# Optimization experiments

Measured on AMD Instinct MI355X. Metric: run time of the kernel, lower is better.

Reference implementation:

```python
import jax, jax.numpy as jnp
import numpy as np

HEADS = 8
DK = 64   # key_size (defaults to size_per_head)
DV = 64   # size_per_head
RATE = 4
OUT = HEADS * DV  # 512


def extract_seq_patches(x, kernel, rate):
    # x: [b, L, d] -> [b, L, kernel, d]; strided local window gather
    b, L, d = x.shape
    k_size = kernel + (rate - 1) * (kernel - 1)
    p_right = (k_size - 1) // 2
    p_left = k_size - 1 - p_right
    xp = jnp.pad(x, ((0, 0), (p_left, p_right), (0, 0)))
    patches = [xp[:, i:i + L] for i in range(0, k_size, rate)]  # kernel slices
    return jnp.stack(patches, axis=2)


def setup_inputs() -> dict:
    key = jax.random.key(0)
    k1, k2, k3, k4 = jax.random.split(key, 4)
    s = 1.0 / np.sqrt(OUT)
    x = jax.random.normal(k1, (2, 4096, OUT), dtype=jnp.float32)
    Wq = jax.random.normal(k2, (OUT, HEADS * DK), dtype=jnp.float32) * s
    Wk = jax.random.normal(k3, (OUT, HEADS * DK), dtype=jnp.float32) * s
    Wv = jax.random.normal(k4, (OUT, HEADS * DV), dtype=jnp.float32) * s
    return {"x": x, "Wq": Wq, "Wk": Wk, "Wv": Wv}


def reference(x, Wq, Wk, Wv):
    b, L, d = x.shape
    pad = RATE - L % RATE  # torch code always pads (pad=RATE when L % RATE == 0)
    xpad = jnp.pad(x, ((0, 0), (0, pad), (0, 0)))
    nL = L + pad
    n = nL // RATE
    kernel = 2 * RATE - 1  # 1 + 2*neighbors

    qw = xpad @ Wq
    kw = xpad @ Wk
    vw = xpad @ Wv

    kwp = extract_seq_patches(kw, kernel, RATE)  # [b, nL, K, H*dk]
    vwp = extract_seq_patches(vw, kernel, RATE)  # [b, nL, K, H*dv]

    # [b, h, r, n, d]
    qw = qw.reshape(b, n, RATE, HEADS, DK).transpose(0, 3, 2, 1, 4)
    kw = kw.reshape(b, n, RATE, HEADS, DK).transpose(0, 3, 2, 1, 4)
    vw = vw.reshape(b, n, RATE, HEADS, DV).transpose(0, 3, 2, 1, 4)
    # [b, h, r, n, K, d]
    kwp = kwp.reshape(b, n, RATE, kernel, HEADS, DK).transpose(0, 4, 2, 1, 3, 5)
    vwp = vwp.reshape(b, n, RATE, kernel, HEADS, DV).transpose(0, 4, 2, 1, 3, 5)

    scale = 1.0 / np.sqrt(DK)
    a = jnp.einsum('bhrnd,bhrmd->bhrnm', qw, kw) * scale    # strided scores [b,h,r,n,n]
    ap = jnp.einsum('bhrnd,bhrnkd->bhrnk', qw, kwp) * scale  # local scores  [b,h,r,n,K]

    A = jax.nn.softmax(jnp.concatenate([a, ap], axis=-1), axis=-1)
    a, ap = A[..., :n], A[..., n:]

    o = jnp.einsum('bhrnm,bhrmd->bhrnd', a, vw) + jnp.einsum('bhrnk,bhrnkd->bhrnd', ap, vwp)
    o = o.transpose(0, 3, 2, 1, 4).reshape(b, nL, HEADS * DV)
    return o[:, :L]
```

## Files before the change

kernel.cpp:

```cpp
#include <hip/hip_runtime.h>
#include <hip/hip_bf16.h>


#define BATCH 2
#define LSEQ  4096
#define DMODEL 512
#define NH    8
#define DHEAD 64
#define NPAD  1088
#define QSCALE 0.18033688011112042f

typedef __bf16 bf16x8 __attribute__((ext_vector_type(8)));
typedef __attribute__((ext_vector_type(4))) float f32x4;
typedef unsigned short u16;
typedef unsigned int u32;
typedef __attribute__((ext_vector_type(8))) u16 u16x8;
typedef __attribute__((ext_vector_type(4))) u16 u16x4;

__device__ __forceinline__ u16 f2bf(float f) {
    u32 u = __float_as_uint(f);
    u += 0x7fffu + ((u >> 16) & 1u);
    return (u16)(u >> 16);
}

__device__ __forceinline__ void gload16(const u16* g, u16* l) {
    __builtin_amdgcn_global_load_lds(
        (const __attribute__((address_space(1))) u32*)(const void*)g,
        (__attribute__((address_space(3))) u32*)(void*)l, 16, 0, 0);
}

__global__ __launch_bounds__(256) void prep_kernel(
    const float* __restrict__ x,
    const float* __restrict__ Wq, const float* __restrict__ Wk, const float* __restrict__ Wv,
    u16* __restrict__ xb, u16* __restrict__ Wt,
    u16* __restrict__ Kb, u16* __restrict__ Vb)
{
    const int bid = blockIdx.x, tid = threadIdx.x;
    if (bid < 2048) {
        const size_t i0 = (size_t)bid * 2048 + (size_t)tid * 8;
        float4 a = *(const float4*)(x + i0);
        float4 b = *(const float4*)(x + i0 + 4);
        u16x8 o = { f2bf(a.x), f2bf(a.y), f2bf(a.z), f2bf(a.w),
                    f2bf(b.x), f2bf(b.y), f2bf(b.z), f2bf(b.w) };
        *(u16x8*)(xb + i0) = o;
    } else if (bid < 2240) {
        const int wb  = bid - 2048;
        const int mat = wb >> 6;
        const int t   = wb & 63;
        const int k0  = (t >> 3) * 64, c0 = (t & 7) * 64;
        const float* W = (mat == 0) ? Wq : (mat == 1) ? Wk : Wv;
        __shared__ u16 Ws[64][72];
        #pragma unroll
        for (int i = 0; i < 4; ++i) {
            const int chunk = i * 256 + tid;
            const int kr = chunk >> 4, c4 = (chunk & 15) * 4;
            float4 v = *(const float4*)(W + (size_t)(k0 + kr) * DMODEL + c0 + c4);
            u16x4 q = { f2bf(v.x), f2bf(v.y), f2bf(v.z), f2bf(v.w) };
            *(u16x4*)&Ws[kr][c4] = q;
        }
        __syncthreads();
        const int cc = tid >> 2, kq = (tid & 3) * 16;
        alignas(16) u16 tmp[16];
        #pragma unroll
        for (int kk = 0; kk < 16; ++kk) tmp[kk] = Ws[kq + kk][cc];
        u16* dst = Wt + (size_t)(mat * 512 + c0 + cc) * DMODEL + k0 + kq;
        *(u16x8*)dst       = *(const u16x8*)&tmp[0];
        *(u16x8*)(dst + 8) = *(const u16x8*)&tmp[8];
    } else {
        const int g = bid - 2240;
        const u16x8 z = {0,0,0,0,0,0,0,0};
        u16* kt = Kb + ((size_t)g * NPAD + 1024) * DHEAD + tid * 16;
        *(u16x8*)kt       = z;
        *(u16x8*)(kt + 8) = z;
        u16* vt = Vb + ((size_t)g * DHEAD + (tid >> 2)) * NPAD + 1024 + (tid & 3) * 16;
        *(u16x8*)vt       = z;
        *(u16x8*)(vt + 8) = z;
    }
}

__global__ __launch_bounds__(256) void gemm_kernel(
    const u16* __restrict__ xb, const u16* __restrict__ Wt,
    u16* __restrict__ Qb, u16* __restrict__ Kb, u16* __restrict__ Vb)
{
    const int m0 = blockIdx.x * 128;
    const int nt = blockIdx.y;
    const int n0 = nt * 128;
    const int tid = threadIdx.x;
    const int w = tid >> 6, l = tid & 63, lr = l & 15, lh = l >> 4;
    const int wr = w >> 1, wc = w & 1;

    __shared__ u16 smem[16896];
    u16* As = smem;
    u16* Bs = smem + 8192;

    f32x4 acc[4][4];
    const f32x4 fzero = {0.f, 0.f, 0.f, 0.f};
    #pragma unroll
    for (int mi = 0; mi < 4; ++mi)
        #pragma unroll
        for (int nj = 0; nj < 4; ++nj) acc[mi][nj] = fzero;

    for (int kt = 0; kt < 8; ++kt) {
        const int k0 = kt * 64;
        #pragma unroll
        for (int i = 0; i < 4; ++i) {
            const int cid = i * 256 + tid;
            const int row = cid >> 3, ch = cid & 7;
            const int sch = ch ^ (row & 7);
            u16* dstA = As + (i * 256 + w * 64) * 8;
            u16* dstB = Bs + (i * 256 + w * 64) * 8;
            gload16(xb + (size_t)(m0 + row) * DMODEL + k0 + sch * 8, dstA);
            gload16(Wt + (size_t)(n0 + row) * DMODEL + k0 + sch * 8, dstB);
        }
        __syncthreads();

        #pragma unroll
        for (int kk = 0; kk < 2; ++kk) {
            const int cs = (kk * 4 + lh) ^ (lr & 7);
            bf16x8 af[4], bfr[4];
            #pragma unroll
            for (int mi = 0; mi < 4; ++mi)
                af[mi] = *(const bf16x8*)(As + (wr * 64 + mi * 16 + lr) * 64 + cs * 8);
            #pragma unroll
            for (int nj = 0; nj < 4; ++nj)
                bfr[nj] = *(const bf16x8*)(Bs + (wc * 64 + nj * 16 + lr) * 64 + cs * 8);
            #pragma unroll
            for (int mi = 0; mi < 4; ++mi)
                #pragma unroll
                for (int nj = 0; nj < 4; ++nj)
                    acc[mi][nj] = __builtin_amdgcn_mfma_f32_16x16x32_bf16(af[mi], bfr[nj], acc[mi][nj], 0, 0, 0);
        }
        __syncthreads();
    }

    const int mat = nt >> 2;
    const int hp  = nt & 3;
    if (mat < 2) {
        u16* Ob = (mat == 0) ? Qb : Kb;
        const float osc = (mat == 0) ? QSCALE : 1.0f;
        #pragma unroll
        for (int mi = 0; mi < 4; ++mi) {
            const int gmb = m0 + wr * 64 + mi * 16 + lh * 4;
            const int b = gmb >> 12;
            #pragma unroll
            for (int rr = 0; rr < 4; ++rr) {
                const int t = (gmb + rr) & 4095;
                const int n = t >> 2, r = t & 3;
                #pragma unroll
                for (int nj = 0; nj < 4; ++nj) {
                    const int c  = wc * 64 + nj * 16 + lr;
                    const int h  = hp * 2 + (c >> 6);
                    const int dk = c & 63;
                    const size_t g = ((size_t)(b * NH + h)) * 4 + r;
                    Ob[(g * NPAD + n) * DHEAD + dk] = f2bf(acc[mi][nj][rr] * osc);
                }
            }
        }
    } else {
        #pragma unroll
        for (int mi = 0; mi < 4; ++mi) {
            const int nrel = wr * 16 + mi * 4 + lh;
            #pragma unroll
            for (int nj = 0; nj < 4; ++nj) {
                const int c = wc * 64 + nj * 16 + lr;
                #pragma unroll
                for (int rr = 0; rr < 4; ++rr)
                    smem[c * 132 + rr * 32 + nrel] = f2bf(acc[mi][nj][rr]);
            }
        }
        __syncthreads();
        const int b  = m0 >> 12;
        const int nb = (m0 & 4095) >> 2;
        #pragma unroll
        for (int e = 0; e < 2; ++e) {
            const int chunk = e * 256 + tid;
            const int c = chunk & 127, r = chunk >> 7;
            const int h  = hp * 2 + (c >> 6);
            const int dv = c & 63;
            const size_t g = ((size_t)(b * NH + h)) * 4 + r;
            u16* dst = Vb + (g * DHEAD + dv) * NPAD + nb;
            const u16* src = smem + c * 132 + r * 32;
            alignas(16) u16 tmp[32];
            #pragma unroll
            for (int q8 = 0; q8 < 8; ++q8)
                *(u16x4*)&tmp[q8 * 4] = *(const u16x4*)(src + q8 * 4);
            #pragma unroll
            for (int q16 = 0; q16 < 4; ++q16)
                *(u16x8*)(dst + q16 * 8) = *(const u16x8*)&tmp[q16 * 8];
        }
    }
}

__global__ __launch_bounds__(512) void attn_kernel(
    const u16* __restrict__ Qb, const u16* __restrict__ Kb, const u16* __restrict__ Vb,
    float* __restrict__ out)
{
    const int g  = blockIdx.x;
    const int b  = g >> 5;
    const int h  = (g >> 2) & 7;
    const int r  = g & 3;
    const int q0 = blockIdx.y * 128;
    const int tid = threadIdx.x;
    const int w  = tid >> 6;
    const int l  = tid & 63;
    const int lr = l & 15, lh = l >> 4;

    const u16* Qg  = Qb + (size_t)g * NPAD * DHEAD;
    const u16* Kg  = Kb + (size_t)g * NPAD * DHEAD;
    const u16* Vtg = Vb + (size_t)g * DHEAD * NPAD;

    __shared__ u16 KV[2][2][4096];
    __shared__ u16 Ps[8][16][68];

    const int srow = tid >> 3;
    const int ssch = (tid & 7) ^ (srow & 7);
    const u16* ksrc0 = Kg  + (size_t)srow * DHEAD + ssch * 8;
    const u16* vsrc0 = Vtg + (size_t)srow * NPAD  + ssch * 8;

    bf16x8 qa[2];
    {
        const u16* qrow = Qg + (size_t)(q0 + w * 16 + lr) * DHEAD;
        qa[0] = *(const bf16x8*)(qrow + lh * 8);
        qa[1] = *(const bf16x8*)(qrow + 32 + lh * 8);
    }

    const f32x4 fzero = {0.f, 0.f, 0.f, 0.f};
    f32x4 o[4];
    #pragma unroll
    for (int j = 0; j < 4; ++j) o[j] = fzero;
    float Lpart[4] = {0.f, 0.f, 0.f, 0.f};

    const int qw0 = q0 + w * 16;

    gload16(ksrc0, &KV[0][0][w * 512]);
    gload16(vsrc0 + 0, &KV[0][1][w * 512]);

    int cur = 0;
    for (int mt = 0; mt < 17; ++mt) {
        if (mt < 16) {
            gload16(ksrc0 + (size_t)(mt + 1) * 4096, &KV[cur ^ 1][0][w * 512]);
            gload16(vsrc0 + (mt + 1) * 64,           &KV[cur ^ 1][1][w * 512]);
            asm volatile("s_waitcnt vmcnt(2)" ::: "memory");
        } else {
            asm volatile("s_waitcnt vmcnt(0)" ::: "memory");
        }
        __builtin_amdgcn_s_barrier();

        const u16* Kbuf = KV[cur][0];
        const u16* Vbuf = KV[cur][1];

        f32x4 s[4];
        #pragma unroll
        for (int ni = 0; ni < 4; ++ni) {
            s[ni] = fzero;
            #pragma unroll
            for (int kk = 0; kk < 2; ++kk) {
                const int slot = (kk * 4 + lh) ^ (lr & 7);
                bf16x8 kb = *(const bf16x8*)(Kbuf + ((ni * 16 + lr) * 8 + slot) * 8);
                s[ni] = __builtin_amdgcn_mfma_f32_16x16x32_bf16(qa[kk], kb, s[ni], 0, 0, 0);
            }
        }

        const int m0 = mt * 64;
        const bool special = (mt == 16) || ((m0 + 66 >= qw0) && (m0 <= qw0 + 18));
        if (!special) {
            #pragma unroll
            for (int ni = 0; ni < 4; ++ni) {
                #pragma unroll
                for (int rr = 0; rr < 4; ++rr) {
                    const float p = __builtin_amdgcn_exp2f(s[ni][rr]);
                    Lpart[rr] += p;
                    Ps[w][lh * 4 + rr][ni * 16 + lr] = f2bf(p);
                }
            }
        } else {
            #pragma unroll
            for (int ni = 0; ni < 4; ++ni) {
                const int mg = m0 + ni * 16 + lr;
                #pragma unroll
                for (int rr = 0; rr < 4; ++rr) {
                    const int qg = qw0 + lh * 4 + rr;
                    float v = s[ni][rr];
                    const int dd = mg - qg;
                    if (mg > 1024)                 v = -1e30f;
                    else if (dd >= -3 && dd <= 3)  v += 1.0f;
                    const float p = __builtin_amdgcn_exp2f(v);
                    Lpart[rr] += p;
                    Ps[w][lh * 4 + rr][ni * 16 + lr] = f2bf(p);
                }
            }
        }

        #pragma unroll
        for (int kk = 0; kk < 2; ++kk) {
            bf16x8 pa = *(const bf16x8*)&Ps[w][lr][kk * 32 + lh * 8];
            #pragma unroll
            for (int j = 0; j < 4; ++j) {
                const int slot = (kk * 4 + lh) ^ (lr & 7);
                bf16x8 vb = *(const bf16x8*)(Vbuf + ((j * 16 + lr) * 8 + slot) * 8);
                o[j] = __builtin_amdgcn_mfma_f32_16x16x32_bf16(pa, vb, o[j], 0, 0, 0);
            }
        }
        __syncthreads();
        cur ^= 1;
    }

    #pragma unroll
    for (int rr = 0; rr < 4; ++rr) {
        float s_ = Lpart[rr];
        #pragma unroll
        for (int off = 1; off < 16; off <<= 1)
            s_ += __shfl_xor(s_, off, 16);
        const int qg = qw0 + lh * 4 + rr;
        const int coob = (qg < 3 ? 3 - qg : 0) + (qg > 1021 ? qg - 1021 : 0);
        const float inv = 1.0f / (s_ + (float)coob);
        const int t = qg * 4 + r;
        float* orow = out + ((size_t)b * LSEQ + t) * DMODEL + h * DHEAD;
        #pragma unroll
        for (int j = 0; j < 4; ++j)
            orow[j * 16 + lr] = o[j][rr] * inv;
    }
}

extern "C" void kernel_launch(void* const* d_in, const int* in_sizes, int n_in,
                              void* d_out, int out_size, void* d_ws, size_t ws_size,
                              hipStream_t stream) {
    const float* x  = (const float*)d_in[0];
    const float* Wq = (const float*)d_in[1];
    const float* Wk = (const float*)d_in[2];
    const float* Wv = (const float*)d_in[3];
    float* out = (float*)d_out;

    const size_t SZ = (size_t)BATCH * NH * 4 * NPAD * DHEAD;
    u16* Qb = (u16*)d_ws;
    u16* Kb = Qb + SZ;
    u16* Vb = Kb + SZ;

    u16* xb = (u16*)d_out;
    u16* Wt = xb + (size_t)8192 * 512;

    prep_kernel<<<2304, 256, 0, stream>>>(x, Wq, Wk, Wv, xb, Wt, Kb, Vb);

    dim3 gg(64, 12);
    gemm_kernel<<<gg, 256, 0, stream>>>(xb, Wt, Qb, Kb, Vb);

    dim3 ga(64, 8);
    attn_kernel<<<ga, 512, 0, stream>>>(Qb, Kb, Vb, out);
}
```

Measured before the change: 67.91 us.

## Drop padded key tile, remap GEMM blocks per XCD, add MFMA priority hints

The attention loop now runs 16 key tiles instead of 17. The padded tail tile is skipped, and its contribution (the zero-key padding columns) is folded into the softmax denominator analytically. This also removes the zero-fill of the K/V pad region from the prep kernel. The GEMM grid is flattened and remapped so that consecutive M tiles land on the same XCD for L2 reuse. Smaller tweaks add s_setprio around the MFMA sections, use hardware bf16 conversion for P, and restructure the QK MFMA chain. The analytic denominator correction for the pad rows must exactly match the reference's zero-padded keys, including the position-4096 padding row.

```diff
diff --git a/kernel.cpp b/kernel.cpp
--- a/kernel.cpp
+++ b/kernel.cpp
@@ -23,6 +23,11 @@
     return (u16)(u >> 16);
 }
 
+__device__ __forceinline__ u16 cvt_bf(float f) {
+    __bf16 t = (__bf16)f;
+    return *(const u16*)&t;
+}
+
 __device__ __forceinline__ void gload16(const u16* g, u16* l) {
     __builtin_amdgcn_global_load_lds(
         (const __attribute__((address_space(1))) u32*)(const void*)g,
@@ -32,8 +37,7 @@
 __global__ __launch_bounds__(256) void prep_kernel(
     const float* __restrict__ x,
     const float* __restrict__ Wq, const float* __restrict__ Wk, const float* __restrict__ Wv,
-    u16* __restrict__ xb, u16* __restrict__ Wt,
-    u16* __restrict__ Kb, u16* __restrict__ Vb)
+    u16* __restrict__ xb, u16* __restrict__ Wt)
 {
     const int bid = blockIdx.x, tid = threadIdx.x;
     if (bid < 2048) {
@@ -43,7 +47,7 @@
         u16x8 o = { f2bf(a.x), f2bf(a.y), f2bf(a.z), f2bf(a.w),
                     f2bf(b.x), f2bf(b.y), f2bf(b.z), f2bf(b.w) };
         *(u16x8*)(xb + i0) = o;
-    } else if (bid < 2240) {
+    } else {
         const int wb  = bid - 2048;
         const int mat = wb >> 6;
         const int t   = wb & 63;
@@ -66,15 +70,6 @@
         u16* dst = Wt + (size_t)(mat * 512 + c0 + cc) * DMODEL + k0 + kq;
         *(u16x8*)dst       = *(const u16x8*)&tmp[0];
         *(u16x8*)(dst + 8) = *(const u16x8*)&tmp[8];
-    } else {
-        const int g = bid - 2240;
-        const u16x8 z = {0,0,0,0,0,0,0,0};
-        u16* kt = Kb + ((size_t)g * NPAD + 1024) * DHEAD + tid * 16;
-        *(u16x8*)kt       = z;
-        *(u16x8*)(kt + 8) = z;
-        u16* vt = Vb + ((size_t)g * DHEAD + (tid >> 2)) * NPAD + 1024 + (tid & 3) * 16;
-        *(u16x8*)vt       = z;
-        *(u16x8*)(vt + 8) = z;
     }
 }
 
@@ -82,8 +77,12 @@
     const u16* __restrict__ xb, const u16* __restrict__ Wt,
     u16* __restrict__ Qb, u16* __restrict__ Kb, u16* __restrict__ Vb)
 {
-    const int m0 = blockIdx.x * 128;
-    const int nt = blockIdx.y;
+    const int bid = blockIdx.x;
+    const int xcd = bid & 7;
+    const int j   = bid >> 3;
+    const int mt  = xcd * 8 + (j / 12);
+    const int nt  = j % 12;
+    const int m0 = mt * 128;
     const int n0 = nt * 128;
     const int tid = threadIdx.x;
     const int w = tid >> 6, l = tid & 63, lr = l & 15, lh = l >> 4;
@@ -233,11 +232,11 @@
     const int qw0 = q0 + w * 16;
 
     gload16(ksrc0, &KV[0][0][w * 512]);
-    gload16(vsrc0 + 0, &KV[0][1][w * 512]);
-
-    int cur = 0;
-    for (int mt = 0; mt < 17; ++mt) {
-        if (mt < 16) {
+    gload16(vsrc0, &KV[0][1][w * 512]);
+
+    for (int mt = 0; mt < 16; ++mt) {
+        const int cur = mt & 1;
+        if (mt < 15) {
             gload16(ksrc0 + (size_t)(mt + 1) * 4096, &KV[cur ^ 1][0][w * 512]);
             gload16(vsrc0 + (mt + 1) * 64,           &KV[cur ^ 1][1][w * 512]);
             asm volatile("s_waitcnt vmcnt(2)" ::: "memory");
@@ -250,19 +249,20 @@
         const u16* Vbuf = KV[cur][1];
 
         f32x4 s[4];
+        __builtin_amdgcn_s_setprio(1);
         #pragma unroll
         for (int ni = 0; ni < 4; ++ni) {
-            s[ni] = fzero;
-            #pragma unroll
-            for (int kk = 0; kk < 2; ++kk) {
-                const int slot = (kk * 4 + lh) ^ (lr & 7);
-                bf16x8 kb = *(const bf16x8*)(Kbuf + ((ni * 16 + lr) * 8 + slot) * 8);
-                s[ni] = __builtin_amdgcn_mfma_f32_16x16x32_bf16(qa[kk], kb, s[ni], 0, 0, 0);
-            }
-        }
+            const int rbase = (ni * 16 + lr) * 8;
+            const int sl0 = lh ^ (lr & 7), sl1 = (4 + lh) ^ (lr & 7);
+            bf16x8 kb0 = *(const bf16x8*)(Kbuf + (rbase + sl0) * 8);
+            bf16x8 kb1 = *(const bf16x8*)(Kbuf + (rbase + sl1) * 8);
+            f32x4 t = __builtin_amdgcn_mfma_f32_16x16x32_bf16(qa[0], kb0, fzero, 0, 0, 0);
+            s[ni] = __builtin_amdgcn_mfma_f32_16x16x32_bf16(qa[1], kb1, t, 0, 0, 0);
+        }
+        __builtin_amdgcn_s_setprio(0);
 
         const int m0 = mt * 64;
-        const bool special = (mt == 16) || ((m0 + 66 >= qw0) && (m0 <= qw0 + 18));
+        const bool special = (m0 + 66 >= qw0) && (m0 <= qw0 + 18);
         if (!special) {
             #pragma unroll
             for (int ni = 0; ni < 4; ++ni) {
@@ -270,7 +270,7 @@
                 for (int rr = 0; rr < 4; ++rr) {
                     const float p = __builtin_amdgcn_exp2f(s[ni][rr]);
                     Lpart[rr] += p;
-                    Ps[w][lh * 4 + rr][ni * 16 + lr] = f2bf(p);
+                    Ps[w][lh * 4 + rr][ni * 16 + lr] = cvt_bf(p);
                 }
             }
         } else {
@@ -282,27 +282,27 @@
                     const int qg = qw0 + lh * 4 + rr;
                     float v = s[ni][rr];
                     const int dd = mg - qg;
-                    if (mg > 1024)                 v = -1e30f;
-                    else if (dd >= -3 && dd <= 3)  v += 1.0f;
+                    if (dd >= -3 && dd <= 3) v += 1.0f;
                     const float p = __builtin_amdgcn_exp2f(v);
                     Lpart[rr] += p;
-                    Ps[w][lh * 4 + rr][ni * 16 + lr] = f2bf(p);
+                    Ps[w][lh * 4 + rr][ni * 16 + lr] = cvt_bf(p);
                 }
             }
         }
 
+        __builtin_amdgcn_s_setprio(1);
         #pragma unroll
         for (int kk = 0; kk < 2; ++kk) {
+            const int slot = (kk * 4 + lh) ^ (lr & 7);
             bf16x8 pa = *(const bf16x8*)&Ps[w][lr][kk * 32 + lh * 8];
             #pragma unroll
             for (int j = 0; j < 4; ++j) {
-                const int slot = (kk * 4 + lh) ^ (lr & 7);
                 bf16x8 vb = *(const bf16x8*)(Vbuf + ((j * 16 + lr) * 8 + slot) * 8);
                 o[j] = __builtin_amdgcn_mfma_f32_16x16x32_bf16(pa, vb, o[j], 0, 0, 0);
             }
         }
-        __syncthreads();
-        cur ^= 1;
+        __builtin_amdgcn_s_setprio(0);
+        __syncthreads();
     }
 
     #pragma unroll
@@ -313,7 +313,8 @@
             s_ += __shfl_xor(s_, off, 16);
         const int qg = qw0 + lh * 4 + rr;
         const int coob = (qg < 3 ? 3 - qg : 0) + (qg > 1021 ? qg - 1021 : 0);
-        const float inv = 1.0f / (s_ + (float)coob);
+        const float extra = (float)(coob + 1 + (qg >= 1021 ? 1 : 0));
+        const float inv = 1.0f / (s_ + extra);
         const int t = qg * 4 + r;
         float* orow = out + ((size_t)b * LSEQ + t) * DMODEL + h * DHEAD;
         #pragma unroll
@@ -339,10 +340,9 @@
     u16* xb = (u16*)d_out;
     u16* Wt = xb + (size_t)8192 * 512;
 
-    prep_kernel<<<2304, 256, 0, stream>>>(x, Wq, Wk, Wv, xb, Wt, Kb, Vb);
-
-    dim3 gg(64, 12);
-    gemm_kernel<<<gg, 256, 0, stream>>>(xb, Wt, Qb, Kb, Vb);
+    prep_kernel<<<2240, 256, 0, stream>>>(x, Wq, Wk, Wv, xb, Wt);
+
+    gemm_kernel<<<768, 256, 0, stream>>>(xb, Wt, Qb, Kb, Vb);
 
     dim3 ga(64, 8);
     attn_kernel<<<ga, 512, 0, stream>>>(Qb, Kb, Vb, out);
```

Measured after the change: 65.43 us. 1.04x faster.
